# Optimization experiments

Measured on AMD Instinct MI355X. Metric: run time of the kernel, lower is better.

## Reference

```python
import jax, jax.numpy as jnp
import numpy as np

B = 8192          # batch
DIM = 2048        # feature dim
FANOUT = 10       # balanced 10-ary tree, depth 3 -> 1000 leaves
N_NODES = 1 + 10 + 100  # inner nodes with classifiers = 111
NUM_CLASSES = 1000


def setup_inputs() -> dict:
    key = jax.random.key(0)
    k1, k2, k3, k4 = jax.random.split(key, 4)
    x = jax.random.normal(k1, (B, DIM), dtype=jnp.float32)
    labels = jax.random.randint(k2, (B,), 0, NUM_CLASSES, dtype=jnp.int64 if jax.config.jax_enable_x64 else jnp.int32)
    # Stacked per-node Linear(dim, num_child+1): column 0 is the extra slot
    # included in the softmax but never routed to (children use cols 1..FANOUT).
    W = jax.random.normal(k3, (N_NODES, DIM, FANOUT + 1), dtype=jnp.float32) * (1.0 / np.sqrt(DIM))
    b = jax.random.normal(k4, (N_NODES, FANOUT + 1), dtype=jnp.float32) * 0.01
    return {"x": x, "labels": labels, "W": W, "b": b}


def reference(x, labels, W, b):
    # All 111 tiny per-node Linear+softmax classifiers fused into one batched GEMM.
    logits = jnp.einsum('bd,ndk->bnk', x, W) + b          # [B, 111, 11]
    probs = jax.nn.softmax(logits, axis=-1)               # softmax over num_child+1 (incl. dummy col 0)
    # Hierarchical path probabilities (root.path_prob = 1.0):
    # level-1 nodes are children of root (node 0), via softmax columns 1..10.
    p1 = probs[:, 0, 1:]                                   # [B, 10]
    # level-2 nodes: children of nodes 1..10
    p2 = (p1[:, :, None] * probs[:, 1:11, 1:]).reshape(x.shape[0], 100)    # [B, 100]
    # leaves: children of nodes 11..110 -> 1000 classes (out[:, 1:] slice already applied)
    out = (p2[:, :, None] * probs[:, 11:111, 1:]).reshape(x.shape[0], NUM_CLASSES)  # [B, 1000]
    penalty = jnp.float32(0.0)
    return (out, penalty)
```

## Files before the change

kernel.cpp:

```cpp
#include <hip/hip_runtime.h>
#include <hip/hip_bf16.h>
#include <hip/hip_fp16.h>

typedef _Float16 f16;
typedef __attribute__((ext_vector_type(8))) _Float16 f16x8;
typedef __attribute__((ext_vector_type(4))) float f32x4;

#define DIM     2048
#define BROWS   8192
#define NCOLS   1221
#define NPAD    1280
#define NNODES  111
#define BM      128
#define BN      128
#define BK      64
#define NKT     (DIM / BK)
#define MT      (BROWS / BM)
#define NT      (NPAD / BN)

__global__ __launch_bounds__(256) void prep_x(const float* __restrict__ X,
                                              f16* __restrict__ Xf) {
    __shared__ float T[128 * 68];
    int blk = blockIdx.x;
    int mt = blk >> 5, kt = blk & 31;
    int t = threadIdx.x;
    int row = t >> 1, half = t & 1;
    const float* src = X + (size_t)(mt * 128 + row) * DIM + kt * 64 + half * 32;
    float* dst = T + row * 68 + half * 32;
    #pragma unroll
    for (int i = 0; i < 8; ++i) ((f32x4*)dst)[i] = ((const f32x4*)src)[i];
    __syncthreads();
    int w = t >> 6, l = t & 63, r = l & 15, q = l >> 4;
    f16* out = Xf + (size_t)blk * 8192;
    #pragma unroll
    for (int p = 0; p < 4; ++p) {
        int gk = p * 4 + w;
        int kk = gk >> 3, g = gk & 7;
        const float* s = T + (g * 16 + r) * 68 + kk * 32 + q * 8;
        f32x4 a = *(const f32x4*)s;
        f32x4 b = *(const f32x4*)(s + 4);
        f16x8 h;
        h[0] = (f16)a[0]; h[1] = (f16)a[1]; h[2] = (f16)a[2]; h[3] = (f16)a[3];
        h[4] = (f16)b[0]; h[5] = (f16)b[1]; h[6] = (f16)b[2]; h[7] = (f16)b[3];
        *(f16x8*)(out + (size_t)(p * 256 + t) * 8) = h;
    }
}

__global__ void prep_b(const float* __restrict__ W, f16* __restrict__ Bf) {
    int idx = blockIdx.x * 256 + threadIdx.x;
    int c = idx & 1023, img = idx >> 10;
    int nt = img >> 5, kt = img & 31;
    int kk = c >> 9, g = (c >> 6) & 7, l = c & 63, r = l & 15, q = l >> 4;
    int col = nt * 128 + g * 16 + r;
    int d0  = kt * 64 + kk * 32 + q * 8;
    f16x8 v;
    if (col < NCOLS) {
        int n = col / 11, k = col - n * 11;
        const float* src = W + ((size_t)n * DIM + d0) * 11 + k;
        #pragma unroll
        for (int e = 0; e < 8; ++e) v[e] = (f16)src[(size_t)e * 11];
    } else {
        #pragma unroll
        for (int e = 0; e < 8; ++e) v[e] = (f16)0.f;
    }
    *(f16x8*)(Bf + (size_t)idx * 8) = v;
}

__global__ __launch_bounds__(512, 4) void gemm_f16(const f16* __restrict__ Xf,
                                                   const f16* __restrict__ Bf,
                                                   f16* __restrict__ Lh) {
    __shared__ __align__(16) f16 As[8192];
    __shared__ __align__(16) f16 Bs[8192];

    int bid = blockIdx.x;
    int swz = (bid & 7) * 80 + (bid >> 3);
    int mt = swz / 10, nt = swz - mt * 10;

    int t = threadIdx.x, w = t >> 6, l = t & 63, r = l & 15, q = l >> 4;
    int wm = w >> 2, wn = w & 3;

    const f16* abase = Xf + (size_t)(mt * 32) * 8192 + (size_t)t * 8;
    const f16* bbase = Bf + (size_t)(nt * 32) * 8192 + (size_t)t * 8;

    f32x4 acc[4][2];
    #pragma unroll
    for (int i = 0; i < 4; ++i)
        #pragma unroll
        for (int j = 0; j < 2; ++j) acc[i][j] = (f32x4)0.f;

    for (int kt = 0; kt < NKT; ++kt) {
        __syncthreads();
        const f16* asrc = abase + (size_t)kt * 8192;
        const f16* bsrc = bbase + (size_t)kt * 8192;
        #pragma unroll
        for (int p = 0; p < 2; ++p) {
            __builtin_amdgcn_global_load_lds(
                (const __attribute__((address_space(1))) void*)(asrc + p * 4096),
                (__attribute__((address_space(3))) void*)(As + p * 4096 + w * 512),
                16, 0, 0);
            __builtin_amdgcn_global_load_lds(
                (const __attribute__((address_space(1))) void*)(bsrc + p * 4096),
                (__attribute__((address_space(3))) void*)(Bs + p * 4096 + w * 512),
                16, 0, 0);
        }
        __syncthreads();
        #pragma unroll
        for (int kk = 0; kk < 2; ++kk) {
            f16x8 af[4], bf[2];
            #pragma unroll
            for (int m = 0; m < 4; ++m)
                af[m] = *(const f16x8*)(As + ((size_t)((kk * 8 + wm * 4 + m) * 64 + l)) * 8);
            #pragma unroll
            for (int n = 0; n < 2; ++n)
                bf[n] = *(const f16x8*)(Bs + ((size_t)((kk * 8 + wn * 2 + n) * 64 + l)) * 8);
            #pragma unroll
            for (int m = 0; m < 4; ++m)
                #pragma unroll
                for (int n = 0; n < 2; ++n)
                    acc[m][n] = __builtin_amdgcn_mfma_f32_16x16x32_f16(af[m], bf[n], acc[m][n], 0, 0, 0);
        }
    }

    #pragma unroll
    for (int m = 0; m < 4; ++m) {
        int row = mt * 128 + wm * 64 + m * 16 + q * 4;
        #pragma unroll
        for (int n = 0; n < 2; ++n) {
            int col = nt * 128 + wn * 32 + n * 16 + r;
            #pragma unroll
            for (int j = 0; j < 4; ++j)
                Lh[(size_t)(row + j) * NPAD + col] = (f16)acc[m][n][j];
        }
    }
}

__global__ void tree_epi(const f16* __restrict__ L, const float* __restrict__ bias,
                         float* __restrict__ out) {
    __shared__ float P[4][NNODES * 11];
    int w = threadIdx.x >> 6, l = threadIdx.x & 63;
    int row = blockIdx.x * 4 + w;
    const f16* Lr = L + (size_t)row * NPAD;

    for (int n = l; n < NNODES; n += 64) {
        float v[11], mx = -1e30f;
        #pragma unroll
        for (int k = 0; k < 11; ++k) { v[k] = (float)Lr[n * 11 + k] + bias[n * 11 + k]; mx = fmaxf(mx, v[k]); }
        float s = 0.f;
        #pragma unroll
        for (int k = 0; k < 11; ++k) { v[k] = __expf(v[k] - mx); s += v[k]; }
        float inv = 1.f / s;
        #pragma unroll
        for (int k = 0; k < 11; ++k) P[w][n * 11 + k] = v[k] * inv;
    }
    __syncthreads();
    const float* Pw = P[w];
    for (int c = l; c < 1000; c += 64) {
        int i  = c / 100;
        int j  = (c % 100) / 10;
        int mm = c % 10;
        float p = Pw[1 + i] * Pw[(1 + i) * 11 + 1 + j] * Pw[(11 + 10 * i + j) * 11 + 1 + mm];
        out[(size_t)row * 1000 + c] = p;
    }
    if (row == 0 && threadIdx.x == 0) out[(size_t)BROWS * 1000] = 0.f;
}

extern "C" void kernel_launch(void* const* d_in, const int* in_sizes, int n_in,
                              void* d_out, int out_size, void* d_ws, size_t ws_size,
                              hipStream_t stream) {
    const float* x    = (const float*)d_in[0];
    const float* W    = (const float*)d_in[2];
    const float* bias = (const float*)d_in[3];
    float* out = (float*)d_out;

    f16* Xf = (f16*)d_ws;
    f16* Bf = (f16*)((char*)d_ws + 33554432);
    f16* Lh = (f16*)((char*)d_ws + 38797312);

    prep_x <<<MT * NKT, 256, 0, stream>>>(x, Xf);
    prep_b <<<1280, 256, 0, stream>>>(W, Bf);
    gemm_f16<<<MT * NT, 512, 0, stream>>>(Xf, Bf, Lh);
    tree_epi<<<BROWS / 4, 256, 0, stream>>>(Lh, bias, out);
}
```

Baseline: 87.62 us.

## Double-buffer GEMM A tiles, load B to registers, merge prep kernels, stage epilogue rows

The two prep kernels are merged into a single launch, which removes one kernel launch. The GEMM now double-buffers the A tile in LDS and prefetches the next k-step with explicit vmcnt waits, so global loads overlap with MFMA work. B fragments are loaded straight into registers, which skips the B shared-memory staging. The tree epilogue copies each logit row into shared memory with vector loads before running the softmax, replacing scattered scalar f16 global reads. In exchange the GEMM uses more registers, depends on hand-written waitcnt ordering, and the B register loads may be less coalesced.

Result: slower. 97.27 us (+11.0%).

```diff
diff --git a/kernel.cpp b/kernel.cpp
--- a/kernel.cpp
+++ b/kernel.cpp
@@ -11,66 +11,65 @@
 #define NCOLS   1221
 #define NPAD    1280
 #define NNODES  111
-#define BM      128
-#define BN      128
 #define BK      64
-#define NKT     (DIM / BK)
-#define MT      (BROWS / BM)
-#define NT      (NPAD / BN)
-
-__global__ __launch_bounds__(256) void prep_x(const float* __restrict__ X,
-                                              f16* __restrict__ Xf) {
+#define NKT     32
+#define IMG     8192
+#define PANEL   (32 * IMG)
+
+__global__ __launch_bounds__(256) void prep_all(const float* __restrict__ X,
+                                                const float* __restrict__ W,
+                                                f16* __restrict__ Xf,
+                                                f16* __restrict__ Bf) {
     __shared__ float T[128 * 68];
-    int blk = blockIdx.x;
-    int mt = blk >> 5, kt = blk & 31;
-    int t = threadIdx.x;
-    int row = t >> 1, half = t & 1;
-    const float* src = X + (size_t)(mt * 128 + row) * DIM + kt * 64 + half * 32;
-    float* dst = T + row * 68 + half * 32;
-    #pragma unroll
-    for (int i = 0; i < 8; ++i) ((f32x4*)dst)[i] = ((const f32x4*)src)[i];
-    __syncthreads();
-    int w = t >> 6, l = t & 63, r = l & 15, q = l >> 4;
-    f16* out = Xf + (size_t)blk * 8192;
-    #pragma unroll
-    for (int p = 0; p < 4; ++p) {
-        int gk = p * 4 + w;
-        int kk = gk >> 3, g = gk & 7;
-        const float* s = T + (g * 16 + r) * 68 + kk * 32 + q * 8;
-        f32x4 a = *(const f32x4*)s;
-        f32x4 b = *(const f32x4*)(s + 4);
-        f16x8 h;
-        h[0] = (f16)a[0]; h[1] = (f16)a[1]; h[2] = (f16)a[2]; h[3] = (f16)a[3];
-        h[4] = (f16)b[0]; h[5] = (f16)b[1]; h[6] = (f16)b[2]; h[7] = (f16)b[3];
-        *(f16x8*)(out + (size_t)(p * 256 + t) * 8) = h;
-    }
-}
-
-__global__ void prep_b(const float* __restrict__ W, f16* __restrict__ Bf) {
-    int idx = blockIdx.x * 256 + threadIdx.x;
-    int c = idx & 1023, img = idx >> 10;
-    int nt = img >> 5, kt = img & 31;
-    int kk = c >> 9, g = (c >> 6) & 7, l = c & 63, r = l & 15, q = l >> 4;
-    int col = nt * 128 + g * 16 + r;
-    int d0  = kt * 64 + kk * 32 + q * 8;
-    f16x8 v;
-    if (col < NCOLS) {
-        int n = col / 11, k = col - n * 11;
-        const float* src = W + ((size_t)n * DIM + d0) * 11 + k;
-        #pragma unroll
-        for (int e = 0; e < 8; ++e) v[e] = (f16)src[(size_t)e * 11];
+    int b = blockIdx.x;
+    if (b < 2048) {
+        int mp = b >> 5, kt = b & 31;
+        int t = threadIdx.x;
+        int row = t >> 1, half = t & 1;
+        const float* src = X + (size_t)(mp * 128 + row) * DIM + kt * 64 + half * 32;
+        float* dst = T + row * 68 + half * 32;
+        #pragma unroll
+        for (int i = 0; i < 8; ++i) ((f32x4*)dst)[i] = ((const f32x4*)src)[i];
+        __syncthreads();
+        int w = t >> 6, l = t & 63, r = l & 15, q = l >> 4;
+        f16* out = Xf + (size_t)b * IMG;
+        #pragma unroll
+        for (int p = 0; p < 4; ++p) {
+            int gk = p * 4 + w;
+            int kk = gk >> 3, g = gk & 7;
+            const float* s = T + (g * 16 + r) * 68 + kk * 32 + q * 8;
+            f32x4 a = *(const f32x4*)s;
+            f32x4 c = *(const f32x4*)(s + 4);
+            f16x8 h;
+            h[0] = (f16)a[0]; h[1] = (f16)a[1]; h[2] = (f16)a[2]; h[3] = (f16)a[3];
+            h[4] = (f16)c[0]; h[5] = (f16)c[1]; h[6] = (f16)c[2]; h[7] = (f16)c[3];
+            *(f16x8*)(out + (size_t)(p * 256 + t) * 8) = h;
+        }
     } else {
-        #pragma unroll
-        for (int e = 0; e < 8; ++e) v[e] = (f16)0.f;
-    }
-    *(f16x8*)(Bf + (size_t)idx * 8) = v;
+        int idx = (b - 2048) * 256 + threadIdx.x;
+        int c = idx & 1023, img = idx >> 10;
+        int np = img >> 5, kt = img & 31;
+        int kk = c >> 9, g = (c >> 6) & 7, l = c & 63, r = l & 15, q = l >> 4;
+        int col = np * 128 + g * 16 + r;
+        int d0  = kt * 64 + kk * 32 + q * 8;
+        f16x8 v;
+        if (col < NCOLS) {
+            int n = col / 11, k = col - n * 11;
+            const float* src = W + ((size_t)n * DIM + d0) * 11 + k;
+            #pragma unroll
+            for (int e = 0; e < 8; ++e) v[e] = (f16)src[(size_t)e * 11];
+        } else {
+            #pragma unroll
+            for (int e = 0; e < 8; ++e) v[e] = (f16)0.f;
+        }
+        *(f16x8*)(Bf + (size_t)idx * 8) = v;
+    }
 }
 
 __global__ __launch_bounds__(512, 4) void gemm_f16(const f16* __restrict__ Xf,
                                                    const f16* __restrict__ Bf,
                                                    f16* __restrict__ Lh) {
-    __shared__ __align__(16) f16 As[8192];
-    __shared__ __align__(16) f16 Bs[8192];
+    __shared__ __align__(16) f16 As[2][8192];
 
     int bid = blockIdx.x;
     int swz = (bid & 7) * 80 + (bid >> 3);
@@ -79,8 +78,8 @@
     int t = threadIdx.x, w = t >> 6, l = t & 63, r = l & 15, q = l >> 4;
     int wm = w >> 2, wn = w & 3;
 
-    const f16* abase = Xf + (size_t)(mt * 32) * 8192 + (size_t)t * 8;
-    const f16* bbase = Bf + (size_t)(nt * 32) * 8192 + (size_t)t * 8;
+    const f16* abase = Xf + (size_t)mt * PANEL + (size_t)t * 8;
+    const f16* bbase = Bf + (size_t)nt * PANEL + (size_t)(wn * 2 * 64 + l) * 8;
 
     f32x4 acc[4][2];
     #pragma unroll
@@ -88,38 +87,71 @@
         #pragma unroll
         for (int j = 0; j < 2; ++j) acc[i][j] = (f32x4)0.f;
 
-    for (int kt = 0; kt < NKT; ++kt) {
-        __syncthreads();
-        const f16* asrc = abase + (size_t)kt * 8192;
-        const f16* bsrc = bbase + (size_t)kt * 8192;
-        #pragma unroll
-        for (int p = 0; p < 2; ++p) {
-            __builtin_amdgcn_global_load_lds(
-                (const __attribute__((address_space(1))) void*)(asrc + p * 4096),
-                (__attribute__((address_space(3))) void*)(As + p * 4096 + w * 512),
-                16, 0, 0);
-            __builtin_amdgcn_global_load_lds(
-                (const __attribute__((address_space(1))) void*)(bsrc + p * 4096),
-                (__attribute__((address_space(3))) void*)(Bs + p * 4096 + w * 512),
-                16, 0, 0);
-        }
-        __syncthreads();
-        #pragma unroll
-        for (int kk = 0; kk < 2; ++kk) {
-            f16x8 af[4], bf[2];
-            #pragma unroll
-            for (int m = 0; m < 4; ++m)
-                af[m] = *(const f16x8*)(As + ((size_t)((kk * 8 + wm * 4 + m) * 64 + l)) * 8);
-            #pragma unroll
-            for (int n = 0; n < 2; ++n)
-                bf[n] = *(const f16x8*)(Bs + ((size_t)((kk * 8 + wn * 2 + n) * 64 + l)) * 8);
-            #pragma unroll
-            for (int m = 0; m < 4; ++m)
-                #pragma unroll
-                for (int n = 0; n < 2; ++n)
-                    acc[m][n] = __builtin_amdgcn_mfma_f32_16x16x32_f16(af[m], bf[n], acc[m][n], 0, 0, 0);
-        }
-    }
+    f16x8 b0[4], b1[4];
+
+#define LOADB(SET, KT)                                                           \
+    { const f16* bp_ = bbase + (size_t)(KT) * 8192;                              \
+      SET[0] = *(const f16x8*)(bp_);                                             \
+      SET[1] = *(const f16x8*)(bp_ + 512);                                       \
+      SET[2] = *(const f16x8*)(bp_ + 4096);                                      \
+      SET[3] = *(const f16x8*)(bp_ + 4608); }
+
+#define STAGE_A(KT, C)                                                           \
+    { const f16* ap_ = abase + (size_t)(KT) * 8192;                              \
+      __builtin_amdgcn_global_load_lds(                                          \
+          (const __attribute__((address_space(1))) void*)(ap_),                  \
+          (__attribute__((address_space(3))) void*)(&As[C][w * 512]), 16, 0, 0); \
+      __builtin_amdgcn_global_load_lds(                                          \
+          (const __attribute__((address_space(1))) void*)(ap_ + 4096),           \
+          (__attribute__((address_space(3))) void*)(&As[C][4096 + w * 512]), 16, 0, 0); }
+
+#define COMPUTE(C, BS)                                                           \
+    { _Pragma("unroll")                                                          \
+      for (int kk = 0; kk < 2; ++kk) {                                           \
+          f16x8 af[4];                                                           \
+          _Pragma("unroll")                                                      \
+          for (int m_ = 0; m_ < 4; ++m_)                                         \
+              af[m_] = *(const f16x8*)(&As[C][((kk * 8 + wm * 4 + m_) * 64 + l) * 8]); \
+          _Pragma("unroll")                                                      \
+          for (int m_ = 0; m_ < 4; ++m_)                                         \
+              _Pragma("unroll")                                                  \
+              for (int n_ = 0; n_ < 2; ++n_)                                     \
+                  acc[m_][n_] = __builtin_amdgcn_mfma_f32_16x16x32_f16(          \
+                      af[m_], BS[kk * 2 + n_], acc[m_][n_], 0, 0, 0);            \
+      } }
+
+#define VM(N)  asm volatile("s_waitcnt vmcnt(" #N ")" ::: "memory")
+#define LGKM0  asm volatile("s_waitcnt lgkmcnt(0)" ::: "memory")
+#define BAR    __builtin_amdgcn_s_barrier()
+
+#define STEP(KT, BCUR, BNXT, CC, CN)                                             \
+    { LOADB(BNXT, (KT) + 1)                                                      \
+      STAGE_A((KT) + 1, CN)                                                      \
+      VM(6);                                                                     \
+      BAR;                                                                       \
+      COMPUTE(CC, BCUR)                                                          \
+      LGKM0;                                                                     \
+      BAR; }
+
+    LOADB(b0, 0)
+    STAGE_A(0, 0)
+
+    for (int kt = 0; kt < 30; kt += 2) {
+        STEP(kt,     b0, b1, 0, 1)
+        STEP(kt + 1, b1, b0, 1, 0)
+    }
+    STEP(30, b0, b1, 0, 1)
+    VM(0);
+    BAR;
+    COMPUTE(1, b1)
+
+#undef LOADB
+#undef STAGE_A
+#undef COMPUTE
+#undef VM
+#undef LGKM0
+#undef BAR
+#undef STEP
 
     #pragma unroll
     for (int m = 0; m < 4; ++m) {
@@ -137,14 +169,20 @@
 __global__ void tree_epi(const f16* __restrict__ L, const float* __restrict__ bias,
                          float* __restrict__ out) {
     __shared__ float P[4][NNODES * 11];
+    __shared__ f16 R[4][NPAD];
     int w = threadIdx.x >> 6, l = threadIdx.x & 63;
     int row = blockIdx.x * 4 + w;
-    const f16* Lr = L + (size_t)row * NPAD;
+
+    const f16x8* src = (const f16x8*)(L + (size_t)row * NPAD);
+    f16x8* dst = (f16x8*)R[w];
+    dst[l]      = src[l];
+    dst[l + 64] = src[l + 64];
+    if (l < 32) dst[l + 128] = src[l + 128];
 
     for (int n = l; n < NNODES; n += 64) {
         float v[11], mx = -1e30f;
         #pragma unroll
-        for (int k = 0; k < 11; ++k) { v[k] = (float)Lr[n * 11 + k] + bias[n * 11 + k]; mx = fmaxf(mx, v[k]); }
+        for (int k = 0; k < 11; ++k) { v[k] = (float)R[w][n * 11 + k] + bias[n * 11 + k]; mx = fmaxf(mx, v[k]); }
         float s = 0.f;
         #pragma unroll
         for (int k = 0; k < 11; ++k) { v[k] = __expf(v[k] - mx); s += v[k]; }
@@ -176,8 +214,7 @@
     f16* Bf = (f16*)((char*)d_ws + 33554432);
     f16* Lh = (f16*)((char*)d_ws + 38797312);
 
-    prep_x <<<MT * NKT, 256, 0, stream>>>(x, Xf);
-    prep_b <<<1280, 256, 0, stream>>>(W, Bf);
-    gemm_f16<<<MT * NT, 512, 0, stream>>>(Xf, Bf, Lh);
+    prep_all<<<2048 + 1280, 256, 0, stream>>>(x, W, Xf, Bf);
+    gemm_f16<<<640, 512, 0, stream>>>(Xf, Bf, Lh);
     tree_epi<<<BROWS / 4, 256, 0, stream>>>(Lh, bias, out);
 }
```
